# Optimization experiments

Measured on AMD Instinct MI355X. Metric: run time of the kernel, lower is better.

Reference implementation:

```python
import jax, jax.numpy as jnp
import numpy as np

NUM_HEADS = 8
NEG_MASK = -1000.0  # original code masks with -1000, not -inf


def setup_inputs() -> dict:
    key = jax.random.key(0)
    ks = jax.random.split(key, 12)
    B, S, D = 4, 2048, 512
    HID, OUT = 512, 512
    dh = D // NUM_HEADS      # 64, per-head input dim
    eh = HID // NUM_HEADS    # 64, per-head hidden dim
    w = 0.02
    return {
        "q": jax.random.normal(ks[0], (B, S, D), dtype=jnp.float32),
        "k": jax.random.normal(ks[1], (B, S, D), dtype=jnp.float32),
        "v": jax.random.normal(ks[2], (B, S, D), dtype=jnp.float32),
        # Linear weights stored as [in, out] (transpose of torch convention)
        "Wq": jax.random.normal(ks[3], (dh, eh), dtype=jnp.float32) * w,
        "bq": jax.random.normal(ks[4], (eh,), dtype=jnp.float32) * w,
        "Wk": jax.random.normal(ks[5], (dh, eh), dtype=jnp.float32) * w,
        "bk": jax.random.normal(ks[6], (eh,), dtype=jnp.float32) * w,
        "Wv": jax.random.normal(ks[7], (dh, eh), dtype=jnp.float32) * w,
        "bv": jax.random.normal(ks[8], (eh,), dtype=jnp.float32) * w,
        "Wo": jax.random.normal(ks[9], (HID, OUT), dtype=jnp.float32) * w,
        "bo": jax.random.normal(ks[10], (OUT,), dtype=jnp.float32) * w,
        "valid_lens": jnp.maximum(jax.random.randint(ks[11], (B,), 0, S), 1),
        "max_len": S,
    }


def reference(q, k, v, Wq, bq, Wk, bk, Wv, bv, Wo, bo, valid_lens, max_len):
    B, S, D = q.shape
    H = NUM_HEADS
    # split into heads: [B, S, H, dh]; note the SAME projection weights are
    # shared across heads (as in the original module)
    qh = q.reshape(B, S, H, D // H)
    kh = k.reshape(B, S, H, D // H)
    vh = v.reshape(B, S, H, D // H)
    qp = jnp.einsum('bshd,de->bshe', qh, Wq) + bq  # [B,S,H,eh]
    kp = jnp.einsum('bshd,de->bshe', kh, Wk) + bk
    vp = jnp.einsum('bshd,de->bshe', vh, Wv) + bv
    scale = 1.0 / jnp.sqrt(jnp.asarray(qp.shape[-1], qp.dtype))
    scores = jnp.einsum('bshe,bthe->bhst', qp, kp) * scale  # [B,H,S,S]
    # key-padding mask: positions j >= valid_len get -1000 (original semantics)
    key_mask = jnp.arange(S)[None, :] < valid_lens[:, None]  # [B,S]
    scores = jnp.where(key_mask[:, None, None, :], scores, NEG_MASK)
    attn = jax.nn.softmax(scores, axis=-1)
    ctx = jnp.einsum('bhst,bthe->bshe', attn, vp).reshape(B, S, -1)  # head-major concat
    return jnp.einsum('bse,eo->bso', ctx, Wo) + bo
```

## Files before the change

kernel.cpp:

```cpp
#include <hip/hip_runtime.h>

#define S_LEN 2048
#define D_MODEL 512

typedef __attribute__((ext_vector_type(8))) short s8v;
typedef __attribute__((ext_vector_type(4))) float f4v;
typedef __attribute__((ext_vector_type(4))) short s4v;
typedef __attribute__((ext_vector_type(4))) int   i4v;
typedef __attribute__((ext_vector_type(2))) int   i2v;

#define MFMA __builtin_amdgcn_mfma_f32_16x16x32_bf16

__device__ inline short f2bf(float x) {
    union { float f; unsigned u; } v; v.f = x;
    unsigned r = v.u + 0x7fffu + ((v.u >> 16) & 1u);
    return (short)(r >> 16);
}
__device__ inline unsigned pack_bf2_trunc(float a, float b) {
    unsigned ua = __builtin_bit_cast(unsigned, a);
    unsigned ub = __builtin_bit_cast(unsigned, b);
    return (ua >> 16) | (ub & 0xffff0000u);
}

template <int C>
__device__ inline float dppf(float x) {
    int i = __builtin_bit_cast(int, x);
    i = __builtin_amdgcn_update_dpp(0, i, C, 0xF, 0xF, true);
    return __builtin_bit_cast(float, i);
}
__device__ inline float rowsum16(float x) {
    x += dppf<0xB1>(x);
    x += dppf<0x4E>(x);
    x += dppf<0x141>(x);
    x += dppf<0x140>(x);
    return x;
}

__global__ __launch_bounds__(256) void prep_kernel(
    const float* __restrict__ Wo, const float* __restrict__ Wq,
    const float* __restrict__ Wk, const float* __restrict__ Wv,
    short* __restrict__ WoT, short* __restrict__ WqT,
    short* __restrict__ WkT, short* __restrict__ WvT)
{
    if (blockIdx.x < 64) {
        __shared__ short t[64 * 65];
        const int bi = (blockIdx.x >> 3) * 64;
        const int bj = (blockIdx.x & 7) * 64;
        const int c = threadIdx.x & 63, rr = threadIdx.x >> 6;
#pragma unroll
        for (int r = 0; r < 16; r++) {
            int i = r * 4 + rr;
            t[c * 65 + i] = f2bf(Wo[(size_t)(bi + i) * 512 + bj + c]);
        }
        __syncthreads();
#pragma unroll
        for (int r = 0; r < 16; r++) {
            int o = r * 4 + rr;
            WoT[(size_t)(bj + o) * 512 + bi + c] = t[o * 65 + c];
        }
    } else {
        for (int j = threadIdx.x; j < 12288; j += 256) {
            int w = j >> 12, r = j & 4095;
            int e = r >> 6, d = r & 63;
            const float* W = (w == 0) ? Wq : (w == 1) ? Wk : Wv;
            short* WT = (w == 0) ? WqT : (w == 1) ? WkT : WvT;
            WT[r] = f2bf(W[d * 64 + e]);
        }
    }
}

__global__ __launch_bounds__(256) void proj_kernel(
    const float* __restrict__ q, const float* __restrict__ k, const float* __restrict__ v,
    const float* __restrict__ bq, const float* __restrict__ bk, const float* __restrict__ bv,
    const short* __restrict__ WqT, const short* __restrict__ WkT, const short* __restrict__ WvT,
    short* __restrict__ qp, short* __restrict__ kp, short* __restrict__ vpT)
{
    const int t = blockIdx.z >> 2;
    const int b = blockIdx.z & 3;
    const int h = blockIdx.y;
    const int qt = blockIdx.x;
    const int w = threadIdx.x >> 6, lane = threadIdx.x & 63;
    const int l = lane & 15, qd = lane >> 4;

    const float* X    = (t == 0) ? q   : (t == 1) ? k   : v;
    const float* bias = (t == 0) ? bq  : (t == 1) ? bk  : bv;
    const short* WT   = (t == 0) ? WqT : (t == 1) ? WkT : WvT;

    const int s0 = qt * 128 + w * 32;

    s8v a[2][2];
#pragma unroll
    for (int mt = 0; mt < 2; mt++)
#pragma unroll
        for (int kk = 0; kk < 2; kk++) {
            const float* p = X + (size_t)(b * S_LEN + s0 + mt * 16 + l) * 512 + h * 64 + kk * 32 + qd * 8;
            f4v x0 = *(const f4v*)p;
            f4v x1 = *(const f4v*)(p + 4);
            s8v fr;
            fr[0] = f2bf(x0[0]); fr[1] = f2bf(x0[1]); fr[2] = f2bf(x0[2]); fr[3] = f2bf(x0[3]);
            fr[4] = f2bf(x1[0]); fr[5] = f2bf(x1[1]); fr[6] = f2bf(x1[2]); fr[7] = f2bf(x1[3]);
            a[mt][kk] = fr;
        }
    s8v wf[4][2];
#pragma unroll
    for (int nt = 0; nt < 4; nt++) {
        int wrow = (t < 2) ? (4 * l + nt) : (nt * 16 + l);
#pragma unroll
        for (int kk = 0; kk < 2; kk++)
            wf[nt][kk] = *(const s8v*)(WT + wrow * 64 + kk * 32 + qd * 8);
    }

    const f4v fz = {0.f, 0.f, 0.f, 0.f};
    f4v acc[2][4];
#pragma unroll
    for (int mt = 0; mt < 2; mt++)
#pragma unroll
        for (int nt = 0; nt < 4; nt++) acc[mt][nt] = fz;

#pragma unroll
    for (int kk = 0; kk < 2; kk++)
#pragma unroll
        for (int nt = 0; nt < 4; nt++)
#pragma unroll
            for (int mt = 0; mt < 2; mt++)
                acc[mt][nt] = MFMA(a[mt][kk], wf[nt][kk], acc[mt][nt], 0, 0, 0);

    const float SC = 0.125f * 1.442695041f;

    if (t < 2) {
        short* out = (t == 0) ? qp : kp;
        float bbs[4];
#pragma unroll
        for (int nt = 0; nt < 4; nt++) bbs[nt] = bias[4 * l + nt];
#pragma unroll
        for (int mt = 0; mt < 2; mt++)
#pragma unroll
            for (int r = 0; r < 4; r++) {
                int s = s0 + mt * 16 + qd * 4 + r;
                s4v pk;
#pragma unroll
                for (int nt = 0; nt < 4; nt++) {
                    float val = acc[mt][nt][r] + bbs[nt];
                    if (t == 0) val *= SC;
                    pk[nt] = f2bf(val);
                }
                *(s4v*)(out + ((size_t)(b * 8 + h) * S_LEN + s) * 64 + 4 * l) = pk;
            }
    } else {
#pragma unroll
        for (int nt = 0; nt < 4; nt++) {
            float bb = bias[nt * 16 + l];
            int e = nt * 16 + l;
#pragma unroll
            for (int mt = 0; mt < 2; mt++) {
                s4v pk;
#pragma unroll
                for (int r = 0; r < 4; r++) pk[r] = f2bf(acc[mt][nt][r] + bb);
                *(s4v*)(vpT + ((size_t)(b * 8 + h) * 64 + e) * S_LEN + s0 + mt * 16 + qd * 4) = pk;
            }
        }
    }
}

__global__ __launch_bounds__(128) void repack_kernel(
    const short* __restrict__ kp, const short* __restrict__ vpT,
    short* __restrict__ kfrag, short* __restrict__ vfrag)
{
    const int kb = blockIdx.x, h = blockIdx.y, b = blockIdx.z;
    const int bh = b * 8 + h;
    const int half = threadIdx.x >> 6, f = threadIdx.x & 63;
    const int l = f & 15, qd = f >> 4;
    const size_t slab = (size_t)bh * S_LEN * 64;
    const size_t obase = ((size_t)bh * 32 + kb) * 4096;
    if (half == 0) {
        const short* src = kp + slab;
#pragma unroll
        for (int c = 0; c < 8; c++) {
            int nt = c >> 1, kk = c & 1;
            s8v x = *(const s8v*)(src + (size_t)(kb * 64 + 4 * l + nt) * 64 + kk * 32 + qd * 8);
            *(s8v*)(kfrag + obase + c * 512 + f * 8) = x;
        }
    } else {
        const short* src = vpT + slab;
#pragma unroll
        for (int c = 0; c < 8; c++) {
            int ne = c >> 1, kk = c & 1;
            s8v x = *(const s8v*)(src + (size_t)(4 * l + ne) * S_LEN + kb * 64 + kk * 32 + qd * 8);
            *(s8v*)(vfrag + obase + c * 512 + f * 8) = x;
        }
    }
}

__global__ __launch_bounds__(128) void attn_kernel(
    const short* __restrict__ qp, const short* __restrict__ kfrag,
    const short* __restrict__ vfrag,
    const int* __restrict__ valid_lens, short* __restrict__ ctx)
{
    __shared__ short lP[2][32 * 72];

    const int gid = blockIdx.x;
    const int h  = gid & 7;
    const int b  = (gid >> 3) & 3;
    const int qt = gid >> 5;
    const int w = threadIdx.x >> 6, lane = threadIdx.x & 63;
    const int l = lane & 15, qd = lane >> 4;
    const int vlen = valid_lens[b];
    const int ntiles = (vlen + 63) >> 6;

    const int bh = b * 8 + h;
    const short* Qs = qp + (size_t)bh * S_LEN * 64;
    const short* Kf = kfrag + (size_t)bh * 32 * 4096;
    const short* Vf = vfrag + (size_t)bh * 32 * 4096;

    const int s0 = qt * 64 + w * 32;
    s8v qf[2][2];
#pragma unroll
    for (int mt = 0; mt < 2; mt++)
#pragma unroll
        for (int kk = 0; kk < 2; kk++)
            qf[mt][kk] = *(const s8v*)(Qs + (size_t)(s0 + mt * 16 + l) * 64 + kk * 32 + qd * 8);

    const f4v fz = {0.f, 0.f, 0.f, 0.f};
    f4v O[2][4];
    float lsum[2][4];
#pragma unroll
    for (int mt = 0; mt < 2; mt++)
#pragma unroll
        for (int r = 0; r < 4; r++) lsum[mt][r] = 0.f;
#pragma unroll
    for (int mt = 0; mt < 2; mt++)
#pragma unroll
        for (int ne = 0; ne < 4; ne++) O[mt][ne] = fz;

    short* lPw = lP[w];

    for (int kb = 0; kb < ntiles; kb++) {
        const short* Kb = Kf + (size_t)kb * 4096 + lane * 8;
        s8v kf[4][2];
#pragma unroll
        for (int nt = 0; nt < 4; nt++)
#pragma unroll
            for (int kk = 0; kk < 2; kk++)
                kf[nt][kk] = *(const s8v*)(Kb + (nt * 2 + kk) * 512);

        f4v sf[2][4];
#pragma unroll
        for (int mt = 0; mt < 2; mt++)
#pragma unroll
            for (int nt = 0; nt < 4; nt++) sf[mt][nt] = fz;
#pragma unroll
        for (int nt = 0; nt < 4; nt++)
#pragma unroll
            for (int mt = 0; mt < 2; mt++) {
                sf[mt][nt] = MFMA(qf[mt][0], kf[nt][0], sf[mt][nt], 0, 0, 0);
                sf[mt][nt] = MFMA(qf[mt][1], kf[nt][1], sf[mt][nt], 0, 0, 0);
            }

        const short* Vb = Vf + (size_t)kb * 4096 + lane * 8;
        s8v vf[4][2];
#pragma unroll
        for (int ne = 0; ne < 4; ne++)
#pragma unroll
            for (int kk = 0; kk < 2; kk++)
                vf[ne][kk] = *(const s8v*)(Vb + (ne * 2 + kk) * 512);

        if (kb == ntiles - 1 && (vlen & 63)) {
            int rem = vlen - kb * 64;
#pragma unroll
            for (int nt = 0; nt < 4; nt++)
                if (4 * l + nt >= rem) {
#pragma unroll
                    for (int mt = 0; mt < 2; mt++)
#pragma unroll
                        for (int r = 0; r < 4; r++) sf[mt][nt][r] = -1e30f;
                }
        }

#pragma unroll
        for (int mt = 0; mt < 2; mt++)
#pragma unroll
            for (int r = 0; r < 4; r++) {
                float p0 = __builtin_amdgcn_exp2f(sf[mt][0][r]);
                float p1 = __builtin_amdgcn_exp2f(sf[mt][1][r]);
                float p2 = __builtin_amdgcn_exp2f(sf[mt][2][r]);
                float p3 = __builtin_amdgcn_exp2f(sf[mt][3][r]);
                lsum[mt][r] += (p0 + p1) + (p2 + p3);
                i2v pk;
                pk[0] = (int)pack_bf2_trunc(p0, p1);
                pk[1] = (int)pack_bf2_trunc(p2, p3);
                *(i2v*)(lPw + (mt * 16 + qd * 4 + r) * 72 + 4 * l) = pk;
            }

        s8v pa[2][2];
#pragma unroll
        for (int mt = 0; mt < 2; mt++)
#pragma unroll
            for (int kk = 0; kk < 2; kk++)
                pa[mt][kk] = *(const s8v*)(lPw + (mt * 16 + l) * 72 + kk * 32 + qd * 8);
#pragma unroll
        for (int ne = 0; ne < 4; ne++)
#pragma unroll
            for (int mt = 0; mt < 2; mt++) {
                O[mt][ne] = MFMA(pa[mt][0], vf[ne][0], O[mt][ne], 0, 0, 0);
                O[mt][ne] = MFMA(pa[mt][1], vf[ne][1], O[mt][ne], 0, 0, 0);
            }
    }

#pragma unroll
    for (int mt = 0; mt < 2; mt++)
#pragma unroll
        for (int r = 0; r < 4; r++) {
            float inv = 1.0f / rowsum16(lsum[mt][r]);
            int s = s0 + mt * 16 + qd * 4 + r;
            s4v pk;
#pragma unroll
            for (int ne = 0; ne < 4; ne++) pk[ne] = f2bf(O[mt][ne][r] * inv);
            *(s4v*)(ctx + ((size_t)(b * S_LEN + s)) * 512 + h * 64 + 4 * l) = pk;
        }
}

__global__ __launch_bounds__(256) void outproj_kernel(
    const short* __restrict__ ctx, const short* __restrict__ WoT,
    const float* __restrict__ bo, float* __restrict__ out)
{
    __shared__ short lB[64 * 520];
    __shared__ short lA[128 * 40];

    const int rb = blockIdx.x * 128;
    const int nb = blockIdx.y * 64;
    const int w = threadIdx.x >> 6, lane = threadIdx.x & 63;
    const int l = lane & 15, qd = lane >> 4;

    {
        int n = threadIdx.x >> 2, c0 = threadIdx.x & 3;
#pragma unroll
        for (int i = 0; i < 16; i++) {
            int g = i * 4 + c0;
            i4v x = *(const i4v*)(WoT + (size_t)(nb + n) * 512 + g * 8);
            *(i4v*)(lB + n * 520 + g * 8) = x;
        }
    }
    __syncthreads();

    const f4v fz = {0.f, 0.f, 0.f, 0.f};
    f4v acc[2][4];
#pragma unroll
    for (int mt = 0; mt < 2; mt++)
#pragma unroll
        for (int nt = 0; nt < 4; nt++) acc[mt][nt] = fz;

    for (int ko = 0; ko < 16; ko++) {
        {
            int r = threadIdx.x >> 1, hp = threadIdx.x & 1;
            const short* src = ctx + (size_t)(rb + r) * 512 + ko * 32 + hp * 16;
            i4v x0 = *(const i4v*)src;
            i4v x1 = *(const i4v*)(src + 8);
            *(i4v*)(lA + r * 40 + hp * 16) = x0;
            *(i4v*)(lA + r * 40 + hp * 16 + 8) = x1;
        }
        __syncthreads();
        s8v af[2];
#pragma unroll
        for (int mt = 0; mt < 2; mt++)
            af[mt] = *(const s8v*)(lA + (w * 32 + mt * 16 + l) * 40 + qd * 8);
#pragma unroll
        for (int nt = 0; nt < 4; nt++) {
            s8v bfr = *(const s8v*)(lB + (nt * 16 + l) * 520 + ko * 32 + qd * 8);
#pragma unroll
            for (int mt = 0; mt < 2; mt++)
                acc[mt][nt] = MFMA(af[mt], bfr, acc[mt][nt], 0, 0, 0);
        }
        __syncthreads();
    }

#pragma unroll
    for (int nt = 0; nt < 4; nt++) {
        float bias = bo[nb + nt * 16 + l];
#pragma unroll
        for (int mt = 0; mt < 2; mt++)
#pragma unroll
            for (int r = 0; r < 4; r++) {
                int row = rb + w * 32 + mt * 16 + qd * 4 + r;
                out[(size_t)row * 512 + nb + nt * 16 + l] = acc[mt][nt][r] + bias;
            }
    }
}

extern "C" void kernel_launch(void* const* d_in, const int* in_sizes, int n_in,
                              void* d_out, int out_size, void* d_ws, size_t ws_size,
                              hipStream_t stream)
{
    const float* q  = (const float*)d_in[0];
    const float* k  = (const float*)d_in[1];
    const float* v  = (const float*)d_in[2];
    const float* Wq = (const float*)d_in[3];
    const float* bq = (const float*)d_in[4];
    const float* Wk = (const float*)d_in[5];
    const float* bk = (const float*)d_in[6];
    const float* Wv = (const float*)d_in[7];
    const float* bv = (const float*)d_in[8];
    const float* Wo = (const float*)d_in[9];
    const float* bo = (const float*)d_in[10];
    const int*   vl = (const int*)d_in[11];
    float* out = (float*)d_out;

    char* ws = (char*)d_ws;
    const size_t SL = (size_t)4 * 8 * S_LEN * 64 * sizeof(short);
    short* qp    = (short*)(ws);
    short* kp    = (short*)(ws + SL);
    short* ctx   = (short*)(ws + SL);
    short* vpT   = (short*)(ws + 2 * SL);
    short* kfrag = (short*)(ws + 3 * SL);
    short* vfrag = (short*)(ws + 4 * SL);
    short* WoT = (short*)(ws + 5 * SL);
    short* WqT = WoT + 512 * 512;
    short* WkT = WqT + 4096;
    short* WvT = WkT + 4096;

    prep_kernel<<<65, 256, 0, stream>>>(Wo, Wq, Wk, Wv, WoT, WqT, WkT, WvT);
    proj_kernel<<<dim3(16, 8, 12), 256, 0, stream>>>(q, k, v, bq, bk, bv,
                                                     WqT, WkT, WvT, qp, kp, vpT);
    repack_kernel<<<dim3(32, 8, 4), 128, 0, stream>>>(kp, vpT, kfrag, vfrag);
    attn_kernel<<<1024, 128, 0, stream>>>(qp, kfrag, vfrag, vl, ctx);
    outproj_kernel<<<dim3(64, 8), 256, 0, stream>>>(ctx, WoT, bo, out);
}
```

Measured before the change: 193.8 us.

## Stage K/V tiles through double-buffered LDS with async global_load_lds in attention

The attention kernel now uses 256-thread blocks covering 128 query rows, so four waves share each K/V tile. Tiles are prefetched one step ahead into double-buffered shared memory with global_load_lds, replacing per-wave direct global loads. This is meant to cut redundant global/L2 traffic and overlap memory latency with MFMA work. The cost is a block-wide barrier every tile, extra LDS use that limits occupancy, and half as many blocks.

```diff
diff --git a/kernel.cpp b/kernel.cpp
--- a/kernel.cpp
+++ b/kernel.cpp
@@ -34,6 +34,12 @@
     x += dppf<0x141>(x);
     x += dppf<0x140>(x);
     return x;
+}
+
+typedef const __attribute__((address_space(1))) void* gptr_t;
+typedef __attribute__((address_space(3))) void* sptr_t;
+__device__ inline void gload16(const void* g, void* s) {
+    __builtin_amdgcn_global_load_lds((gptr_t)g, (sptr_t)s, 16, 0, 0);
 }
 
 __global__ __launch_bounds__(256) void prep_kernel(
@@ -191,12 +197,14 @@
     }
 }
 
-__global__ __launch_bounds__(128) void attn_kernel(
+__global__ __launch_bounds__(256, 3) void attn_kernel(
     const short* __restrict__ qp, const short* __restrict__ kfrag,
     const short* __restrict__ vfrag,
     const int* __restrict__ valid_lens, short* __restrict__ ctx)
 {
-    __shared__ short lP[2][32 * 72];
+    __shared__ alignas(16) short kbuf[2][4096];
+    __shared__ alignas(16) short vbuf[2][4096];
+    __shared__ alignas(16) short lP[4][32 * 72];
 
     const int gid = blockIdx.x;
     const int h  = gid & 7;
@@ -212,7 +220,7 @@
     const short* Kf = kfrag + (size_t)bh * 32 * 4096;
     const short* Vf = vfrag + (size_t)bh * 32 * 4096;
 
-    const int s0 = qt * 64 + w * 32;
+    const int s0 = qt * 128 + w * 32;
     s8v qf[2][2];
 #pragma unroll
     for (int mt = 0; mt < 2; mt++)
@@ -233,9 +241,26 @@
         for (int ne = 0; ne < 4; ne++) O[mt][ne] = fz;
 
     short* lPw = lP[w];
+    const int toff = threadIdx.x * 8;
+
+    gload16(Kf + toff,        &kbuf[0][toff]);
+    gload16(Kf + 2048 + toff, &kbuf[0][2048 + toff]);
+    gload16(Vf + toff,        &vbuf[0][toff]);
+    gload16(Vf + 2048 + toff, &vbuf[0][2048 + toff]);
+    __syncthreads();
 
     for (int kb = 0; kb < ntiles; kb++) {
-        const short* Kb = Kf + (size_t)kb * 4096 + lane * 8;
+        const int cur = kb & 1;
+        if (kb + 1 < ntiles) {
+            const short* Ks = Kf + (size_t)(kb + 1) * 4096;
+            const short* Vs = Vf + (size_t)(kb + 1) * 4096;
+            gload16(Ks + toff,        &kbuf[cur ^ 1][toff]);
+            gload16(Ks + 2048 + toff, &kbuf[cur ^ 1][2048 + toff]);
+            gload16(Vs + toff,        &vbuf[cur ^ 1][toff]);
+            gload16(Vs + 2048 + toff, &vbuf[cur ^ 1][2048 + toff]);
+        }
+
+        const short* Kb = &kbuf[cur][lane * 8];
         s8v kf[4][2];
 #pragma unroll
         for (int nt = 0; nt < 4; nt++)
@@ -256,7 +281,7 @@
                 sf[mt][nt] = MFMA(qf[mt][1], kf[nt][1], sf[mt][nt], 0, 0, 0);
             }
 
-        const short* Vb = Vf + (size_t)kb * 4096 + lane * 8;
+        const short* Vb = &vbuf[cur][lane * 8];
         s8v vf[4][2];
 #pragma unroll
         for (int ne = 0; ne < 4; ne++)
@@ -304,6 +329,8 @@
                 O[mt][ne] = MFMA(pa[mt][0], vf[ne][0], O[mt][ne], 0, 0, 0);
                 O[mt][ne] = MFMA(pa[mt][1], vf[ne][1], O[mt][ne], 0, 0, 0);
             }
+
+        __syncthreads();
     }
 
 #pragma unroll
@@ -421,6 +448,6 @@
     proj_kernel<<<dim3(16, 8, 12), 256, 0, stream>>>(q, k, v, bq, bk, bv,
                                                      WqT, WkT, WvT, qp, kp, vpT);
     repack_kernel<<<dim3(32, 8, 4), 128, 0, stream>>>(kp, vpT, kfrag, vfrag);
-    attn_kernel<<<1024, 128, 0, stream>>>(qp, kfrag, vfrag, vl, ctx);
+    attn_kernel<<<512, 256, 0, stream>>>(qp, kfrag, vfrag, vl, ctx);
     outproj_kernel<<<dim3(64, 8), 256, 0, stream>>>(ctx, WoT, bo, out);
 }
```

After: 185.9 us. 1.04x faster.
